# Optimization experiments

Hardware: AMD Instinct MI355X
Metric: run time of the kernel (lower is better)

## Reference

```python
import jax, jax.numpy as jnp
import numpy as np

TOPK = 13
NUM_CLASSES = 20
ALPHA = 1.0
BETA = 6.0
EPS = 1e-9
B, N, A, C = 16, 64, 8400, NUM_CLASSES


def _ciou(box1, box2, eps=1e-7):
    """CIoU between broadcastable xyxy boxes (ultralytics bbox_iou, CIoU=True)."""
    b1x1, b1y1, b1x2, b1y2 = box1[..., 0], box1[..., 1], box1[..., 2], box1[..., 3]
    b2x1, b2y1, b2x2, b2y2 = box2[..., 0], box2[..., 1], box2[..., 2], box2[..., 3]
    w1, h1 = b1x2 - b1x1, b1y2 - b1y1
    w2, h2 = b2x2 - b2x1, b2y2 - b2y1
    inter = (jnp.minimum(b1x2, b2x2) - jnp.maximum(b1x1, b2x1)).clip(0) * \
            (jnp.minimum(b1y2, b2y2) - jnp.maximum(b1y1, b2y1)).clip(0)
    union = w1 * h1 + w2 * h2 - inter + eps
    iou = inter / union
    cw = jnp.maximum(b1x2, b2x2) - jnp.minimum(b1x1, b2x1)  # enclosing box
    ch = jnp.maximum(b1y2, b2y2) - jnp.minimum(b1y1, b2y1)
    c2 = cw * cw + ch * ch + eps
    rho2 = ((b2x1 + b2x2 - b1x1 - b1x2) ** 2 + (b2y1 + b2y2 - b1y1 - b1y2) ** 2) / 4.0
    v = (4.0 / (np.pi ** 2)) * (jnp.arctan(w2 / (h2 + eps)) - jnp.arctan(w1 / (h1 + eps))) ** 2
    alpha = v / (v - iou + (1.0 + eps))
    return iou - (rho2 / c2 + v * alpha)


def _make_boxes(key, shape):
    k1, k2 = jax.random.split(key)
    cxy = jax.random.uniform(k1, shape + (2,)) * 608.0 + 16.0
    wh = jax.random.uniform(k2, shape + (2,)) * 110.0 + 10.0
    return jnp.concatenate([cxy - wh / 2, cxy + wh / 2], axis=-1)


def setup_inputs() -> dict:
    key = jax.random.key(0)
    ks = jax.random.split(key, 6)
    pd_scores = jax.random.uniform(ks[0], (B, A, C), dtype=jnp.float32)
    pd_bboxes = _make_boxes(ks[1], (B, A))
    anc_points = jax.random.uniform(ks[2], (A, 2), dtype=jnp.float32) * 640.0
    gt_labels = jax.random.randint(ks[3], (B, N, 1), 0, C, dtype=jnp.int64)
    gt_bboxes = _make_boxes(ks[4], (B, N))
    mask_gt = jnp.broadcast_to((jnp.arange(N) < 48).astype(jnp.float32)[None, :, None], (B, N, 1))
    return {"pd_scores": pd_scores, "pd_bboxes": pd_bboxes, "anc_points": anc_points,
            "gt_labels": gt_labels, "gt_bboxes": gt_bboxes, "mask_gt": mask_gt}


def reference(pd_scores, pd_bboxes, anc_points, gt_labels, gt_bboxes, mask_gt):
    # --- select_candidates_in_gts: anchor center inside gt box, [B,N,A] bool ---
    lt = gt_bboxes[:, :, None, :2]                      # [B,N,1,2]
    rb = gt_bboxes[:, :, None, 2:]                      # [B,N,1,2]
    anc = anc_points[None, None, :, :]                  # [1,1,A,2]
    d = jnp.minimum(jnp.minimum((anc - lt)[..., 0], (anc - lt)[..., 1]),
                    jnp.minimum((rb - anc)[..., 0], (rb - anc)[..., 1]))
    mask_in_gts = d > 1e-9                              # [B,N,A]

    mask_valid = mask_in_gts & (mask_gt > 0)            # [B,N,A] (mask_gt broadcasts)

    # --- get_box_metrics ---
    pdt = jnp.swapaxes(pd_scores, 1, 2)                 # [B,C,A]
    lbl = jnp.broadcast_to(gt_labels, (B, N, A))        # [B,N,A]
    scores = jnp.take_along_axis(pdt, lbl, axis=1)      # pd_scores[b,:,label] -> [B,N,A]
    bbox_scores = jnp.where(mask_valid, scores, 0.0)
    ciou = _ciou(gt_bboxes[:, :, None, :], pd_bboxes[:, None, :, :]).clip(0.0)
    overlaps = jnp.where(mask_valid, ciou, 0.0)         # [B,N,A]
    align_metric = (bbox_scores ** ALPHA) * (overlaps ** BETA)

    # --- select_topk_candidates ---
    _, topk_idxs = jax.lax.top_k(align_metric, TOPK)    # [B,N,TOPK]
    mask_topk = jnp.zeros((B, N, A), jnp.float32).at[
        jnp.arange(B)[:, None, None], jnp.arange(N)[None, :, None], topk_idxs].set(1.0)

    mask_pos = mask_topk * mask_in_gts.astype(jnp.float32) * mask_gt  # [B,N,A]

    # --- select_highest_overlaps (unconditional form; identical when no conflicts) ---
    fg_mask = mask_pos.sum(axis=1)                      # [B,A]
    mask_multi = fg_mask[:, None, :] > 1                # [B,1,A]
    max_idx = jnp.argmax(overlaps, axis=1)              # [B,A]
    is_max = jnp.arange(N)[None, :, None] == max_idx[:, None, :]
    non_overlaps = jnp.where(mask_multi & ~is_max, 0.0, 1.0)
    mask_pos = mask_pos * non_overlaps
    fg_mask = mask_pos.sum(axis=1)
    target_gt_idx = jnp.argmax(mask_pos, axis=1)        # [B,A]

    # --- get_targets ---
    target_labels = jnp.take_along_axis(gt_labels[:, :, 0], target_gt_idx, axis=1)  # [B,A]
    target_bboxes = jnp.take_along_axis(
        gt_bboxes, jnp.broadcast_to(target_gt_idx[..., None], (B, A, 4)), axis=1)   # [B,A,4]
    target_labels = jnp.clip(target_labels, 0)
    fg = fg_mask > 0                                    # [B,A] bool
    target_scores = jax.nn.one_hot(target_labels, NUM_CLASSES, dtype=jnp.float32)
    target_scores = target_scores * fg[..., None]

    # --- normalization of target scores ---
    align_metric = align_metric * mask_pos
    pos_align = align_metric.max(axis=-1, keepdims=True)              # [B,N,1]
    pos_ov = (overlaps * mask_pos).max(axis=-1, keepdims=True)        # [B,N,1]
    norm = (align_metric * pos_ov / (pos_align + EPS)).max(axis=1)[..., None]  # [B,A,1]
    target_scores = target_scores * norm

    return (target_labels, target_bboxes, target_scores, fg, target_gt_idx)
```

## Files before the change

kernel.cpp:

```cpp
#include <hip/hip_runtime.h>
#include <hip/hip_bf16.h>

#define BB 16
#define NN 64
#define AA 8400
#define CC 20
#define TOPKK 13
#define NG 33
#define SEGCAP 48
#define ROWCAP 128

__device__ __forceinline__ int inside_pt(float gx1, float gy1, float gx2, float gy2,
                                         float ax, float ay) {
    float d = fminf(fminf(ax - gx1, ay - gy1), fminf(gx2 - ax, gy2 - ay));
    return d > 1e-9f;
}

__device__ __forceinline__ float atan_wh4(float4 b) {
    return atanf((b.z - b.x) / ((b.w - b.y) + 1e-7f));
}

__device__ __forceinline__ float ciou_clip(float4 g, float4 p, float at_p, float at_g) {
    const float eps = 1e-7f;
    float w1 = g.z - g.x, h1 = g.w - g.y;
    float w2 = p.z - p.x, h2 = p.w - p.y;
    float ix = fmaxf(fminf(g.z, p.z) - fmaxf(g.x, p.x), 0.0f);
    float iy = fmaxf(fminf(g.w, p.w) - fmaxf(g.y, p.y), 0.0f);
    float inter = ix * iy;
    float uni = w1 * h1 + w2 * h2 - inter + eps;
    float iou = inter / uni;
    float cw = fmaxf(g.z, p.z) - fminf(g.x, p.x);
    float ch = fmaxf(g.w, p.w) - fminf(g.y, p.y);
    float c2 = cw * cw + ch * ch + eps;
    float dx = p.x + p.z - g.x - g.z;
    float dy = p.y + p.w - g.y - g.w;
    float rho2 = (dx * dx + dy * dy) * 0.25f;
    float at = at_p - at_g;
    float v = 0.40528473456935109f * (at * at);
    float alpha = v / (v - iou + 1.0000001f);
    return fmaxf(iou - (rho2 / c2 + v * alpha), 0.0f);
}

__device__ __forceinline__ unsigned long long pack_ov(float ov, int n) {
    return ((unsigned long long)__float_as_uint(ov) << 6) | (unsigned)(63 - n);
}
__device__ __forceinline__ int unpack_n(unsigned long long k) {
    return 63 - (int)(k & 63ull);
}

__global__ __launch_bounds__(256) void k1_scan(
    const float* __restrict__ pd_scores, const float4* __restrict__ pd_bboxes,
    const float2* __restrict__ anc, const int* __restrict__ gt_labels, int lab_stride,
    const float4* __restrict__ gt_bboxes, const float* __restrict__ mask_gt,
    unsigned long long* __restrict__ pos_bits, unsigned long long* __restrict__ winner,
    int* __restrict__ cnt,
    float* __restrict__ g_val, float* __restrict__ g_ov, int* __restrict__ g_ai,
    float4* __restrict__ out_scores4)
{
    __shared__ float4 lds_gt[NN];
    __shared__ float  lds_atg[NN];
    __shared__ int    lds_lab[NN];
    __shared__ int    lds_cnt[NN];

    const int tid  = threadIdx.x;
    const int gtid = blockIdx.x * 256 + tid;
    const int lane = tid & 63;
    const int NTH  = BB * NG * 256;

    if (gtid < BB * AA) pos_bits[gtid] = 0ull;
    float4 z4 = make_float4(0.f, 0.f, 0.f, 0.f);
    for (int i = gtid; i < BB * AA * 5; i += NTH) out_scores4[i] = z4;

    const int b    = blockIdx.x / NG;
    const int grp  = blockIdx.x - b * NG;
    const int rowb = b * NN;

    if (tid < NN) {
        float4 g4 = gt_bboxes[rowb + tid];
        lds_gt[tid]  = g4;
        lds_atg[tid] = atan_wh4(g4);
        int lab = gt_labels[(rowb + tid) * lab_stride];
        lds_lab[tid] = (mask_gt[rowb + tid] > 0.0f) ? lab : -1;
        lds_cnt[tid] = 0;
    }
    __syncthreads();

    unsigned long long vmask = __ballot(lds_lab[lane] >= 0);

    int a = grp * 256 + tid;
    bool va = a < AA;
    float2 ap = va ? anc[a] : make_float2(-1e9f, -1e9f);
    float4 p  = va ? pd_bboxes[(size_t)b * AA + a] : make_float4(0.f, 0.f, 0.f, 1.f);
    float atp = atan_wh4(p);
    const float* psb = pd_scores + ((size_t)b * AA + a) * CC;

    unsigned long long im = 0ull;
    if (va) {
        unsigned long long m = vmask;
        while (m) {
            int n = __ffsll((unsigned long long)m) - 1;
            m &= m - 1;
            float4 g4 = lds_gt[n];
            if (inside_pt(g4.x, g4.y, g4.z, g4.w, ap.x, ap.y)) im |= 1ull << n;
        }
    }

    unsigned long long wmax = pack_ov(0.0f, 0);
    unsigned long long m = im;
    while (m) {
        int n = __ffsll((unsigned long long)m) - 1;
        m &= m - 1;
        float4 g4 = lds_gt[n];
        float ov = ciou_clip(g4, p, atp, lds_atg[n]);
        unsigned long long key = pack_ov(ov, n);
        if (key > wmax) wmax = key;
        float o2 = ov * ov;
        float al = psb[lds_lab[n]] * (o2 * o2 * o2);
        if (al > 0.0f) {
            int slot = atomicAdd(&lds_cnt[n], 1);
            if (slot < SEGCAP) {
                size_t o = ((size_t)(rowb + n) * NG + grp) * SEGCAP + slot;
                g_val[o] = al; g_ov[o] = ov; g_ai[o] = a;
            }
        }
    }
    if (va) winner[(size_t)b * AA + a] = wmax;

    __syncthreads();
    if (tid < NN) cnt[(size_t)(rowb + tid) * NG + grp] = min(lds_cnt[tid], SEGCAP);
}

__global__ __launch_bounds__(256) void k2_topk(
    const float* __restrict__ pd_scores, const float4* __restrict__ pd_bboxes,
    const float2* __restrict__ anc, const int* __restrict__ gt_labels, int lab_stride,
    const float4* __restrict__ gt_bboxes, const float* __restrict__ mask_gt,
    const int* __restrict__ cnt,
    const float* __restrict__ g_val, const float* __restrict__ g_ov,
    const int* __restrict__ g_ai,
    unsigned long long* __restrict__ pos_bits,
    int* __restrict__ cand_idx, float* __restrict__ cand_ov,
    float* __restrict__ cand_al, int* __restrict__ cand_cnt)
{
    __shared__ unsigned short smap[4][ROWCAP];
    const int tid  = threadIdx.x;
    const int lane = tid & 63;
    const int wid  = tid >> 6;
    const int r    = blockIdx.x * 4 + wid;
    const int b = r >> 6, n = r & 63;

    float mg = mask_gt[r];
    bool active = mg > 0.0f;

    int c = 0;
    if (active && lane < NG) c = cnt[(size_t)r * NG + lane];
    int incl = c;
    #pragma unroll
    for (int off = 1; off < 64; off <<= 1) {
        int y = __shfl_up(incl, off);
        if (lane >= off) incl += y;
    }
    int excl = incl - c;
    int p_all = __shfl(incl, 63);

    if (active) {
        for (int k = 0; k < c; ++k) {
            int q = excl + k;
            if (q < ROWCAP) smap[wid][q] = (unsigned short)((lane << 6) | k);
        }
    }
    __syncthreads();

    int p = min(p_all, ROWCAP);
    float v0 = -1.0f, v1 = -1.0f, ovr0 = 0.0f, ovr1 = 0.0f;
    int a0 = 1 << 30, a1 = 1 << 30;
    if (active) {
        if (lane < p) {
            int m = smap[wid][lane]; int w = m >> 6, k = m & 63;
            size_t o = ((size_t)r * NG + w) * SEGCAP + k;
            v0 = g_val[o]; ovr0 = g_ov[o]; a0 = g_ai[o];
        }
        if (lane + 64 < p) {
            int m = smap[wid][lane + 64]; int w = m >> 6, k = m & 63;
            size_t o = ((size_t)r * NG + w) * SEGCAP + k;
            v1 = g_val[o]; ovr1 = g_ov[o]; a1 = g_ai[o];
        }
    }
    int nr = active ? min(p, TOPKK) : 0;
    for (int k = 0; k < nr; ++k) {
        float bv; int ba; float bo;
        if (v0 > v1 || (v0 == v1 && a0 < a1)) { bv = v0; ba = a0; bo = ovr0; }
        else                                   { bv = v1; ba = a1; bo = ovr1; }
        #pragma unroll
        for (int s2 = 32; s2 > 0; s2 >>= 1) {
            float v2 = __shfl_xor(bv, s2);
            int   aa2 = __shfl_xor(ba, s2);
            float o2 = __shfl_xor(bo, s2);
            if (v2 > bv || (v2 == bv && aa2 < ba)) { bv = v2; ba = aa2; bo = o2; }
        }
        if (lane == 0) {
            cand_idx[r * TOPKK + k] = ba;
            cand_ov[r * TOPKK + k]  = bo;
            cand_al[r * TOPKK + k]  = bv;
            atomicOr(&pos_bits[(size_t)b * AA + ba], 1ull << n);
        }
        if (a0 == ba) v0 = -1.0f;
        if (a1 == ba) v1 = -1.0f;
    }

    int nsel_final;
    if (active && p < TOPKK) {
        int st = 1; float so = 0.0f;
        if (lane < 32) {
            float4 g4 = gt_bboxes[r];
            float2 apx = anc[lane];
            int ins = inside_pt(g4.x, g4.y, g4.z, g4.w, apx.x, apx.y);
            float o = 0.0f, al = 0.0f;
            if (ins) {
                float4 pp = pd_bboxes[(size_t)b * AA + lane];
                o = ciou_clip(g4, pp, atan_wh4(pp), atan_wh4(g4));
                int label = gt_labels[r * lab_stride];
                float sc = pd_scores[((size_t)b * AA + lane) * CC + label];
                float o2 = o * o;
                al = sc * (o2 * o2 * o2);
            }
            so = o;
            st = (al == 0.0f) ? (ins ? 2 : 1) : 0;
        }
        int nsel = nr, need = TOPKK - p;
        for (int a2 = 0; a2 < 32; ++a2) {
            int sta = __shfl(st, a2);
            float oa = __shfl(so, a2);
            if (lane == 0 && need > 0 && sta != 0) {
                if (sta == 2) {
                    cand_idx[r * TOPKK + nsel] = a2;
                    cand_ov[r * TOPKK + nsel]  = oa;
                    cand_al[r * TOPKK + nsel]  = 0.0f;
                    atomicOr(&pos_bits[(size_t)b * AA + a2], 1ull << n);
                    nsel++;
                }
                need--;
            }
        }
        nsel_final = nsel;
    } else {
        nsel_final = active ? nr : 0;
    }
    if (lane == 0) {
        cand_cnt[r] = nsel_final;
        for (int j = nsel_final; j < TOPKK; ++j) {
            cand_idx[r * TOPKK + j] = 0;
            cand_ov[r * TOPKK + j]  = 0.0f;
            cand_al[r * TOPKK + j]  = 0.0f;
        }
    }
}

__global__ __launch_bounds__(256) void k3_out(
    const unsigned long long* __restrict__ pos_bits,
    const unsigned long long* __restrict__ winner,
    const int* __restrict__ gt_labels, int lab_stride,
    const float4* __restrict__ gt_bboxes,
    const int* __restrict__ cand_idx, const float* __restrict__ cand_ov,
    const float* __restrict__ cand_al, const int* __restrict__ cand_cnt,
    float* __restrict__ out_labels, float* __restrict__ out_bboxes,
    float* __restrict__ out_scores, float* __restrict__ out_fg,
    float* __restrict__ out_tgt)
{
    int i = blockIdx.x * 256 + threadIdx.x;
    if (i >= BB * AA) return;
    int b = i / AA, a = i - b * AA;

    unsigned long long bits = pos_bits[i];
    unsigned long long wi   = winner[i];
    if (__popcll(bits) > 1) bits &= (1ull << unpack_n(wi));

    int fg = bits != 0ull;
    int tgt = fg ? (__ffsll((unsigned long long)bits) - 1) : 0;
    int row = b * NN + tgt;
    int label = gt_labels[row * lab_stride];
    label = label > 0 ? label : 0;
    float4 g = gt_bboxes[row];
    out_labels[i] = (float)label;
    ((float4*)out_bboxes)[i] = g;

    if (fg) {
        int cntn = cand_cnt[row];
        float al = 0.0f, pa = 0.0f, po = 0.0f;
        #pragma unroll
        for (int j = 0; j < TOPKK; ++j) {
            int aj   = cand_idx[row * TOPKK + j];
            float cal = cand_al[row * TOPKK + j];
            float cov = cand_ov[row * TOPKK + j];
            size_t oj = (size_t)b * AA + aj;
            unsigned long long bj = pos_bits[oj];
            unsigned long long wj = winner[oj];
            bool valid = j < cntn;
            if (__popcll(bj) > 1) bj &= (1ull << unpack_n(wj));
            if (valid && ((bj >> tgt) & 1ull)) {
                pa = fmaxf(pa, cal);
                po = fmaxf(po, cov);
            }
            if (valid && aj == a) al = cal;
        }
        float norm = (al * po) / (pa + 1e-9f);
        out_scores[(size_t)i * CC + label] = norm;
    }
    out_fg[i] = fg ? 1.0f : 0.0f;
    out_tgt[i] = (float)tgt;
}

extern "C" void kernel_launch(void* const* d_in, const int* in_sizes, int n_in,
                              void* d_out, int out_size, void* d_ws, size_t ws_size,
                              hipStream_t stream) {
    const float*  pd_scores = (const float*)d_in[0];
    const float4* pd_bboxes = (const float4*)d_in[1];
    const float2* anc       = (const float2*)d_in[2];
    const int*    gt_labels = (const int*)d_in[3];
    const float4* gt_bboxes = (const float4*)d_in[4];
    const float*  mask_gt   = (const float*)d_in[5];
    int lab_stride = (in_sizes[3] == 2 * BB * NN) ? 2 : 1;

    const int BA = BB * AA;
    const int BN = BB * NN;

    char* ws = (char*)d_ws;
    size_t off = 0;
    unsigned long long* pos_bits = (unsigned long long*)(ws + off); off += (size_t)BA * 8;
    unsigned long long* winner   = (unsigned long long*)(ws + off); off += (size_t)BA * 8;
    int*   cnt      = (int*)(ws + off);    off += (size_t)BN * NG * 4;
    float* g_val    = (float*)(ws + off);  off += (size_t)BN * NG * SEGCAP * 4;
    float* g_ov     = (float*)(ws + off);  off += (size_t)BN * NG * SEGCAP * 4;
    int*   g_ai     = (int*)(ws + off);    off += (size_t)BN * NG * SEGCAP * 4;
    int*   cand_idx = (int*)(ws + off);    off += (size_t)BN * TOPKK * 4;
    float* cand_ov  = (float*)(ws + off);  off += (size_t)BN * TOPKK * 4;
    float* cand_al  = (float*)(ws + off);  off += (size_t)BN * TOPKK * 4;
    int*   cand_cnt = (int*)(ws + off);

    float* out_labels = (float*)d_out;
    float* out_bboxes = out_labels + BA;
    float* out_scores = out_bboxes + (size_t)BA * 4;
    float* out_fg     = out_scores + (size_t)BA * CC;
    float* out_tgt    = out_fg + BA;

    k1_scan<<<BB * NG, 256, 0, stream>>>(
        pd_scores, pd_bboxes, anc, gt_labels, lab_stride, gt_bboxes, mask_gt,
        pos_bits, winner, cnt, g_val, g_ov, g_ai, (float4*)out_scores);
    k2_topk<<<BN / 4, 256, 0, stream>>>(
        pd_scores, pd_bboxes, anc, gt_labels, lab_stride, gt_bboxes, mask_gt,
        cnt, g_val, g_ov, g_ai, pos_bits, cand_idx, cand_ov, cand_al, cand_cnt);
    k3_out<<<(BA + 255) / 256, 256, 0, stream>>>(
        pos_bits, winner, gt_labels, lab_stride, gt_bboxes,
        cand_idx, cand_ov, cand_al, cand_cnt,
        out_labels, out_bboxes, out_scores, out_fg, out_tgt);
}
```

Before: 35.70 us.

## Fuse output kernel into top-k kernel via last-block-per-batch counter

Removes the separate output kernel launch. Each k2 block atomically increments a per-batch done counter after a threadfence, and the last of the 16 blocks for a batch then writes all outputs for that batch's anchors. This saves a launch and its inter-kernel gap, but the output phase now runs on only 16 blocks serially looping over 8400 anchors instead of spreading across the whole GPU.

Result: slower. 104.4 us (+192.4%).

```diff
diff --git a/kernel.cpp b/kernel.cpp
--- a/kernel.cpp
+++ b/kernel.cpp
@@ -55,7 +55,7 @@
     unsigned long long* __restrict__ pos_bits, unsigned long long* __restrict__ winner,
     int* __restrict__ cnt,
     float* __restrict__ g_val, float* __restrict__ g_ov, int* __restrict__ g_ai,
-    float4* __restrict__ out_scores4)
+    float4* __restrict__ out_scores4, int* __restrict__ done)
 {
     __shared__ float4 lds_gt[NN];
     __shared__ float  lds_atg[NN];
@@ -68,6 +68,7 @@
     const int NTH  = BB * NG * 256;
 
     if (gtid < BB * AA) pos_bits[gtid] = 0ull;
+    if (gtid < BB) done[gtid] = 0;
     float4 z4 = make_float4(0.f, 0.f, 0.f, 0.f);
     for (int i = gtid; i < BB * AA * 5; i += NTH) out_scores4[i] = z4;
 
@@ -130,7 +131,7 @@
     if (tid < NN) cnt[(size_t)(rowb + tid) * NG + grp] = min(lds_cnt[tid], SEGCAP);
 }
 
-__global__ __launch_bounds__(256) void k2_topk(
+__global__ __launch_bounds__(256) void k2_fused(
     const float* __restrict__ pd_scores, const float4* __restrict__ pd_bboxes,
     const float2* __restrict__ anc, const int* __restrict__ gt_labels, int lab_stride,
     const float4* __restrict__ gt_bboxes, const float* __restrict__ mask_gt,
@@ -138,15 +139,22 @@
     const float* __restrict__ g_val, const float* __restrict__ g_ov,
     const int* __restrict__ g_ai,
     unsigned long long* __restrict__ pos_bits,
+    const unsigned long long* __restrict__ winner,
     int* __restrict__ cand_idx, float* __restrict__ cand_ov,
-    float* __restrict__ cand_al, int* __restrict__ cand_cnt)
+    float* __restrict__ cand_al, int* __restrict__ cand_cnt,
+    int* __restrict__ done,
+    float* __restrict__ out_labels, float* __restrict__ out_bboxes,
+    float* __restrict__ out_scores, float* __restrict__ out_fg,
+    float* __restrict__ out_tgt)
 {
     __shared__ unsigned short smap[4][ROWCAP];
+    __shared__ int s_last;
     const int tid  = threadIdx.x;
     const int lane = tid & 63;
     const int wid  = tid >> 6;
     const int r    = blockIdx.x * 4 + wid;
     const int b = r >> 6, n = r & 63;
+    const int batch = blockIdx.x >> 4;
 
     float mg = mask_gt[r];
     bool active = mg > 0.0f;
@@ -253,60 +261,57 @@
             cand_al[r * TOPKK + j]  = 0.0f;
         }
     }
-}
-
-__global__ __launch_bounds__(256) void k3_out(
-    const unsigned long long* __restrict__ pos_bits,
-    const unsigned long long* __restrict__ winner,
-    const int* __restrict__ gt_labels, int lab_stride,
-    const float4* __restrict__ gt_bboxes,
-    const int* __restrict__ cand_idx, const float* __restrict__ cand_ov,
-    const float* __restrict__ cand_al, const int* __restrict__ cand_cnt,
-    float* __restrict__ out_labels, float* __restrict__ out_bboxes,
-    float* __restrict__ out_scores, float* __restrict__ out_fg,
-    float* __restrict__ out_tgt)
-{
-    int i = blockIdx.x * 256 + threadIdx.x;
-    if (i >= BB * AA) return;
-    int b = i / AA, a = i - b * AA;
-
-    unsigned long long bits = pos_bits[i];
-    unsigned long long wi   = winner[i];
-    if (__popcll(bits) > 1) bits &= (1ull << unpack_n(wi));
-
-    int fg = bits != 0ull;
-    int tgt = fg ? (__ffsll((unsigned long long)bits) - 1) : 0;
-    int row = b * NN + tgt;
-    int label = gt_labels[row * lab_stride];
-    label = label > 0 ? label : 0;
-    float4 g = gt_bboxes[row];
-    out_labels[i] = (float)label;
-    ((float4*)out_bboxes)[i] = g;
-
-    if (fg) {
-        int cntn = cand_cnt[row];
-        float al = 0.0f, pa = 0.0f, po = 0.0f;
-        #pragma unroll
-        for (int j = 0; j < TOPKK; ++j) {
-            int aj   = cand_idx[row * TOPKK + j];
-            float cal = cand_al[row * TOPKK + j];
-            float cov = cand_ov[row * TOPKK + j];
-            size_t oj = (size_t)b * AA + aj;
-            unsigned long long bj = pos_bits[oj];
-            unsigned long long wj = winner[oj];
-            bool valid = j < cntn;
-            if (__popcll(bj) > 1) bj &= (1ull << unpack_n(wj));
-            if (valid && ((bj >> tgt) & 1ull)) {
-                pa = fmaxf(pa, cal);
-                po = fmaxf(po, cov);
+
+    __syncthreads();
+    if (tid == 0) {
+        __threadfence();
+        int old = atomicAdd(&done[batch], 1);
+        s_last = (old == 15);
+    }
+    __syncthreads();
+    if (!s_last) return;
+    __threadfence();
+
+    for (int a = tid; a < AA; a += 256) {
+        size_t i = (size_t)batch * AA + a;
+        unsigned long long bits = pos_bits[i];
+        unsigned long long wi   = winner[i];
+        if (__popcll(bits) > 1) bits &= (1ull << unpack_n(wi));
+
+        int fg = bits != 0ull;
+        int tgt = fg ? (__ffsll((unsigned long long)bits) - 1) : 0;
+        int row = batch * NN + tgt;
+        int label = gt_labels[row * lab_stride];
+        label = label > 0 ? label : 0;
+        float4 g = gt_bboxes[row];
+        out_labels[i] = (float)label;
+        ((float4*)out_bboxes)[i] = g;
+
+        if (fg) {
+            int cntn = cand_cnt[row];
+            float al = 0.0f, pa = 0.0f, po = 0.0f;
+            #pragma unroll
+            for (int j = 0; j < TOPKK; ++j) {
+                int aj   = cand_idx[row * TOPKK + j];
+                float cal = cand_al[row * TOPKK + j];
+                float cov = cand_ov[row * TOPKK + j];
+                size_t oj = (size_t)batch * AA + aj;
+                unsigned long long bj = pos_bits[oj];
+                unsigned long long wj = winner[oj];
+                bool valid = j < cntn;
+                if (__popcll(bj) > 1) bj &= (1ull << unpack_n(wj));
+                if (valid && ((bj >> tgt) & 1ull)) {
+                    pa = fmaxf(pa, cal);
+                    po = fmaxf(po, cov);
+                }
+                if (valid && aj == a) al = cal;
             }
-            if (valid && aj == a) al = cal;
-        }
-        float norm = (al * po) / (pa + 1e-9f);
-        out_scores[(size_t)i * CC + label] = norm;
-    }
-    out_fg[i] = fg ? 1.0f : 0.0f;
-    out_tgt[i] = (float)tgt;
+            float norm = (al * po) / (pa + 1e-9f);
+            out_scores[i * CC + label] = norm;
+        }
+        out_fg[i] = fg ? 1.0f : 0.0f;
+        out_tgt[i] = (float)tgt;
+    }
 }
 
 extern "C" void kernel_launch(void* const* d_in, const int* in_sizes, int n_in,
@@ -334,7 +339,8 @@
     int*   cand_idx = (int*)(ws + off);    off += (size_t)BN * TOPKK * 4;
     float* cand_ov  = (float*)(ws + off);  off += (size_t)BN * TOPKK * 4;
     float* cand_al  = (float*)(ws + off);  off += (size_t)BN * TOPKK * 4;
-    int*   cand_cnt = (int*)(ws + off);
+    int*   cand_cnt = (int*)(ws + off);    off += (size_t)BN * 4;
+    int*   done     = (int*)(ws + off);
 
     float* out_labels = (float*)d_out;
     float* out_bboxes = out_labels + BA;
@@ -344,12 +350,10 @@
 
     k1_scan<<<BB * NG, 256, 0, stream>>>(
         pd_scores, pd_bboxes, anc, gt_labels, lab_stride, gt_bboxes, mask_gt,
-        pos_bits, winner, cnt, g_val, g_ov, g_ai, (float4*)out_scores);
-    k2_topk<<<BN / 4, 256, 0, stream>>>(
+        pos_bits, winner, cnt, g_val, g_ov, g_ai, (float4*)out_scores, done);
+    k2_fused<<<BN / 4, 256, 0, stream>>>(
         pd_scores, pd_bboxes, anc, gt_labels, lab_stride, gt_bboxes, mask_gt,
-        cnt, g_val, g_ov, g_ai, pos_bits, cand_idx, cand_ov, cand_al, cand_cnt);
-    k3_out<<<(BA + 255) / 256, 256, 0, stream>>>(
-        pos_bits, winner, gt_labels, lab_stride, gt_bboxes,
-        cand_idx, cand_ov, cand_al, cand_cnt,
+        cnt, g_val, g_ov, g_ai, pos_bits, winner,
+        cand_idx, cand_ov, cand_al, cand_cnt, done,
         out_labels, out_bboxes, out_scores, out_fg, out_tgt);
 }
```
